# Performance work log

Hardware: AMD Instinct MI355X
Metric: run time of the kernel (lower is better)

## Reference

```python
import jax, jax.numpy as jnp
import numpy as np
from functools import partial

B, L, V = 64, 512, 20000
P, M = 150, 6          # total patterns, max pattern length
NEG = -1e9             # semiring zero (log-space)
END_STATES = np.repeat(np.array([3, 4, 5]), 50)  # pattern_len-1 per pattern


@jax.custom_vjp
def ste_heaviside(x):
    return (x > 0).astype(x.dtype)

def _ste_fwd(x):
    return ste_heaviside(x), None

def _ste_bwd(_, g):
    return (g,)  # straight-through identity (matches torch code path)

ste_heaviside.defvjp(_ste_fwd, _ste_bwd)


def setup_inputs() -> dict:
    key = jax.random.key(0)
    ks = jax.random.split(key, 8)
    return {
        "docs": jax.random.randint(ks[0], (B, L), 0, V),
        "doc_lens": jax.random.randint(ks[1], (B,), 1, L),
        "local_embeddings": jax.random.normal(ks[2], (300, V), jnp.float32),
        "diags": jax.random.normal(ks[3], (P * M, 300), jnp.float32) * 0.05,
        "bias": jax.random.normal(ks[4], (P * M, 1), jnp.float32) * 0.05,
        "wildcards": jax.random.normal(ks[5], (P, M - 1), jnp.float32) * 0.05,
        "ln_gamma": jnp.ones((P,), jnp.float32),
        "ln_beta": jnp.zeros((P,), jnp.float32),
        "linear_w": jax.random.normal(ks[6], (2, P), jnp.float32) * 0.05,
        "linear_b": jnp.zeros((2,), jnp.float32),
    }


def reference(docs, doc_lens, local_embeddings, diags, bias, wildcards,
              ln_gamma, ln_beta, linear_w, linear_b):
    end_states = jnp.asarray(END_STATES)                  # [P]
    pat_idx = jnp.arange(P)

    # transition matrices over local vocab, mapped into log-space semiring
    tm_vocab = jax.nn.log_sigmoid((diags @ local_embeddings + bias).T)  # [V, P*M]
    tm = tm_vocab[docs].reshape(B, L, P, M)               # [B,L,P,M]

    # wildcard transitions: semiring.times(one=0, log_sigmoid(wildcards))
    wild = jax.nn.log_sigmoid(wildcards)                  # [P, M-1]

    restart = jnp.zeros((B, P, 1), tm.dtype)              # semiring one
    hid0 = jnp.full((B, P, M), NEG, tm.dtype).at[:, :, 0].set(0.0)
    scores0 = jnp.full((B, P), NEG, tm.dtype)             # semiring zero

    def step(carry, inputs):
        hid, sc = carry
        t, tm_t = inputs                                  # tm_t: [B,P,M]
        main = jnp.concatenate([restart, hid[:, :, :-1] + tm_t[:, :, :-1]], axis=2)
        wildp = jnp.concatenate([restart, hid[:, :, :-1] + wild[None]], axis=2)
        hid = jnp.maximum(main, wildp)                    # semiring plus
        esv = hid[:, pat_idx, end_states]                 # [B,P]
        active = (doc_lens > t)[:, None]
        sc = jnp.where(active, jnp.maximum(sc, esv), sc)
        return (hid, sc), None

    xs = (jnp.arange(L), jnp.moveaxis(tm, 1, 0))          # [L], [L,B,P,M]
    (_, scores), _ = jax.lax.scan(step, (hid0, scores0), xs)

    scores = jnp.exp(scores)                              # from_semiring_to_outer
    mu = scores.mean(axis=-1, keepdims=True)
    var = scores.var(axis=-1, keepdims=True)
    norm = (scores - mu) * jax.lax.rsqrt(var + 1e-5) * ln_gamma + ln_beta
    binar = ste_heaviside(norm)
    return binar @ linear_w.T + linear_b
```

## Files before the change

### kernel.cpp

```cpp
#include <hip/hip_runtime.h>
#include <hip/hip_bf16.h>
#include <hip/hip_fp16.h>
#include <math.h>

#define B_   64
#define L_   512
#define V_   20000
#define P_   150
#define M_   6
#define KDIM 300
#define NOUT 750
#define CWS  752
#define NEGF (-1.0e9f)

#define BM 128
#define BN 128
#define BK 16
#define LDP 132

#define KP 320
#define NIT 10
#define NVG 157
#define NJ  6
#define TILE_U4 1024
#define SA 1024.0f
#define SB 16384.0f
#define INV24 (5.9604644775390625e-8f)

#define TCHUNK 32
#define NCHUNK (L_ / TCHUNK)
#define WARM   5
#define CS_STRIDE 160

typedef _Float16 f16x8 __attribute__((ext_vector_type(8)));
typedef float f32x16 __attribute__((ext_vector_type(16)));

__device__ __forceinline__ float logsigf(float x) {
    return fminf(x, 0.f) - log1pf(expf(-fabsf(x)));
}

__device__ __forceinline__ float logsigf_fast(float x) {
    return fminf(x, 0.f) - __logf(1.f + __expf(-fabsf(x)));
}

__device__ __forceinline__ void gload_lds16(const void* gp, void* lp) {
    __builtin_amdgcn_global_load_lds(
        (const __attribute__((address_space(1))) unsigned int*)gp,
        (__attribute__((address_space(3))) unsigned int*)lp, 16, 0, 0);
}


__global__ __launch_bounds__(256) void p1_split_a(
    const float* __restrict__ emb, uint4* __restrict__ a_t)
{
    __shared__ float T[64][132];
    const int t  = threadIdx.x;
    const int gx = blockIdx.x;
    const int ky = blockIdx.y;
    const int v0 = gx * 128;
    const int k0 = ky * 64;

    #pragma unroll
    for (int pass = 0; pass < 8; ++pass) {
        int flat = pass * 256 + t;
        int krow = flat >> 5;
        int c4   = (flat & 31) * 4;
        int kg   = k0 + krow;
        int v    = v0 + c4;
        float4 f = {0.f, 0.f, 0.f, 0.f};
        if (kg < KDIM && v + 3 < V_)
            f = *(const float4*)(emb + (size_t)kg * V_ + v);
        *(float4*)&T[krow][c4] = f;
    }
    __syncthreads();

    const int vv = t >> 1;
    const int kh = (t & 1) * 32;
    const int it = ky * 2 + (kh >> 5);
    const int v  = v0 + vv;
    if (v < V_) {
        union { ushort u[8]; uint4 q; } H[4], Lo[4];
        #pragma unroll
        for (int i = 0; i < 32; ++i) {
            float x = T[kh + i][vv] * SA;
            __half h = __float2half_rn(x);
            float rem = x - __half2float(h);
            H[i >> 3].u[i & 7]  = __half_as_ushort(h);
            Lo[i >> 3].u[i & 7] = __half_as_ushort(__float2half_rn(rem));
        }
        uint4* tile = a_t + ((size_t)gx * NIT + it) * TILE_U4;
        #pragma unroll
        for (int c = 0; c < 4; ++c) {
            tile[      c * 128 + vv] = H[c].q;
            tile[512 + c * 128 + vv] = Lo[c].q;
        }
    }
}

__global__ __launch_bounds__(256) void p2_split_b(
    const float* __restrict__ diags, uint4* __restrict__ b_t)
{
    const int bidx = blockIdx.x;
    const int it   = bidx % NIT;
    const int j    = bidx / NIT;
    const int t    = threadIdx.x;
    const int row  = t >> 1;
    const int qh   = (t & 1) * 2;
    const int n    = j * 128 + row;
    const bool nok = (n < NOUT);
    const int pm   = nok ? ((n / 5) * 6 + (n % 5)) : 0;
    uint4* tile = b_t + (size_t)bidx * TILE_U4;
    #pragma unroll
    for (int qq = 0; qq < 2; ++qq) {
        int q = qh + qq;
        union { ushort u[8]; uint4 v; } H, Lo;
        #pragma unroll
        for (int e = 0; e < 8; ++e) {
            int k = it * 32 + q * 8 + e;
            float x = (nok && k < KDIM) ? diags[(size_t)pm * KDIM + k] * SB : 0.f;
            __half h = __float2half_rn(x);
            float rem = x - __half2float(h);
            H.u[e]  = __half_as_ushort(h);
            Lo.u[e] = __half_as_ushort(__float2half_rn(rem));
        }
        tile[      q * 128 + row] = H.v;
        tile[512 + q * 128 + row] = Lo.v;
    }
}

__global__ __launch_bounds__(256, 3) void k1m_gemm(
    const uint4* __restrict__ a_t, const uint4* __restrict__ b_t,
    const float* __restrict__ bias, const float* __restrict__ wildc,
    float* __restrict__ cw)
{
    const int bid  = blockIdx.x;
    const int xcd  = bid & 7;
    const int slot = bid >> 3;
    const int g    = xcd + 8 * (slot / 6);
    const int j    = slot % 6;
    if (g >= NVG) return;

    __shared__ uint4 sm[4 * 512];
    const int t    = threadIdx.x;
    const int lane = t & 63;
    const int w    = t >> 6;
    const int wr   = w >> 1, wc = w & 1;
    const int v0   = g * 128;
    const int n0   = j * 128;

    const uint4* gsec = (w < 2)
        ? a_t + (size_t)g * NIT * TILE_U4 + w * 512
        : b_t + (size_t)j * NIT * TILE_U4 + (w - 2) * 512;

    const int fk16 = lane >> 5;
    const int fm   = lane & 31;

    f32x16 acc[2][2];
    #pragma unroll
    for (int i = 0; i < 2; ++i)
        #pragma unroll
        for (int jj = 0; jj < 2; ++jj)
            #pragma unroll
            for (int r = 0; r < 16; ++r) acc[i][jj][r] = 0.f;

    for (int it = 0; it < NIT; ++it) {
        const uint4* gp = gsec + (size_t)it * TILE_U4 + lane;
        #pragma unroll
        for (int i = 0; i < 8; ++i)
            gload_lds16(gp + i * 64, &sm[w * 512 + i * 64 + lane]);
        __syncthreads();

        #pragma unroll
        for (int s = 0; s < 2; ++s) {
            f16x8 A1[2], A2[2], B1[2], B2[2];
            const int q = s * 2 + fk16;
            #pragma unroll
            for (int ri = 0; ri < 2; ++ri) {
                A1[ri] = *(const f16x8*)&sm[(0 * 4 + q) * 128 + wr * 64 + ri * 32 + fm];
                A2[ri] = *(const f16x8*)&sm[(1 * 4 + q) * 128 + wr * 64 + ri * 32 + fm];
            }
            #pragma unroll
            for (int cj = 0; cj < 2; ++cj) {
                B1[cj] = *(const f16x8*)&sm[(2 * 4 + q) * 128 + wc * 64 + cj * 32 + fm];
                B2[cj] = *(const f16x8*)&sm[(3 * 4 + q) * 128 + wc * 64 + cj * 32 + fm];
            }
            #pragma unroll
            for (int ri = 0; ri < 2; ++ri)
                #pragma unroll
                for (int cj = 0; cj < 2; ++cj) {
                    acc[ri][cj] = __builtin_amdgcn_mfma_f32_32x32x16_f16(A1[ri], B1[cj], acc[ri][cj], 0, 0, 0);
                    acc[ri][cj] = __builtin_amdgcn_mfma_f32_32x32x16_f16(A1[ri], B2[cj], acc[ri][cj], 0, 0, 0);
                    acc[ri][cj] = __builtin_amdgcn_mfma_f32_32x32x16_f16(A2[ri], B1[cj], acc[ri][cj], 0, 0, 0);
                }
        }
        __syncthreads();
    }

    float biasv[2], lwv[2]; int ncol[2]; bool nok[2];
    #pragma unroll
    for (int cj = 0; cj < 2; ++cj) {
        int n = n0 + wc * 64 + cj * 32 + fm;
        ncol[cj] = n;
        nok[cj]  = (n < NOUT);
        int nc = nok[cj] ? n : 0;
        int pm = (nc / 5) * 6 + (nc % 5);
        biasv[cj] = bias[pm];
        lwv[cj]   = logsigf_fast(wildc[nc]);
    }
    #pragma unroll
    for (int ri = 0; ri < 2; ++ri) {
        int vbase = v0 + wr * 64 + ri * 32 + 4 * fk16;
        #pragma unroll
        for (int cj = 0; cj < 2; ++cj) {
            if (!nok[cj]) continue;
            #pragma unroll
            for (int r = 0; r < 16; ++r) {
                int v = vbase + (r & 3) + 8 * (r >> 2);
                if (v < V_) {
                    float val = acc[ri][cj][r] * INV24 + biasv[cj];
                    cw[(size_t)v * CWS + ncol[cj]] = fmaxf(logsigf_fast(val), lwv[cj]);
                }
            }
        }
    }
}


__global__ __launch_bounds__(256) void k1_gemm_cw(
    const float* __restrict__ emb,
    const float* __restrict__ diags,
    const float* __restrict__ bias,
    const float* __restrict__ wildc,
    float* __restrict__ cw)
{
    __shared__ float As[BK][LDP];
    __shared__ float Bs[BK][LDP];

    const int tid = threadIdx.x;
    const int v0 = blockIdx.x * BM;
    const int n0 = blockIdx.y * BN;
    const int tx = tid & 15;
    const int ty = tid >> 4;

    float acc[8][8];
    #pragma unroll
    for (int i = 0; i < 8; ++i)
        #pragma unroll
        for (int j = 0; j < 8; ++j) acc[i][j] = 0.f;

    const int a_k = tid >> 4;
    const int a_v = (tid & 15) * 8;
    const int b_n   = tid >> 1;
    const int b_kof = (tid & 1) * 8;

    int  brow;
    bool bval;
    {
        int n = n0 + b_n;
        bval = (n < NOUT);
        brow = bval ? ((n / 5) * 6 + (n % 5)) : 0;
    }

    for (int k0 = 0; k0 < KDIM; k0 += BK) {
        {
            float4 f0 = {0,0,0,0}, f1 = {0,0,0,0};
            int k = k0 + a_k;
            if (k < KDIM) {
                const float* src = emb + (size_t)k * V_ + v0 + a_v;
                if (v0 + a_v + 3 < V_) f0 = *(const float4*)src;
                if (v0 + a_v + 7 < V_) f1 = *(const float4*)(src + 4);
            }
            *(float4*)&As[a_k][a_v]     = f0;
            *(float4*)&As[a_k][a_v + 4] = f1;
        }
        {
            float4 f = {0,0,0,0}, g = {0,0,0,0};
            if (bval) {
                const float* src = diags + (size_t)brow * KDIM + k0 + b_kof;
                if (k0 + b_kof + 3 < KDIM) f = *(const float4*)src;
                if (k0 + b_kof + 7 < KDIM) g = *(const float4*)(src + 4);
            }
            Bs[b_kof + 0][b_n] = f.x;
            Bs[b_kof + 1][b_n] = f.y;
            Bs[b_kof + 2][b_n] = f.z;
            Bs[b_kof + 3][b_n] = f.w;
            Bs[b_kof + 4][b_n] = g.x;
            Bs[b_kof + 5][b_n] = g.y;
            Bs[b_kof + 6][b_n] = g.z;
            Bs[b_kof + 7][b_n] = g.w;
        }
        __syncthreads();
        #pragma unroll
        for (int k = 0; k < BK; ++k) {
            float4 a0 = *(const float4*)&As[k][tx * 4];
            float4 a1 = *(const float4*)&As[k][64 + tx * 4];
            float4 b0 = *(const float4*)&Bs[k][ty * 8];
            float4 b1 = *(const float4*)&Bs[k][ty * 8 + 4];
            float av[8] = {a0.x, a0.y, a0.z, a0.w, a1.x, a1.y, a1.z, a1.w};
            float bv[8] = {b0.x, b0.y, b0.z, b0.w, b1.x, b1.y, b1.z, b1.w};
            #pragma unroll
            for (int i = 0; i < 8; ++i)
                #pragma unroll
                for (int j = 0; j < 8; ++j)
                    acc[i][j] = fmaf(av[i], bv[j], acc[i][j]);
        }
        __syncthreads();
    }

    float biasv[8], lwv[8];
    #pragma unroll
    for (int j = 0; j < 8; ++j) {
        int n  = n0 + ty * 8 + j;
        int nc = (n < NOUT) ? n : 0;
        int pm = (nc / 5) * 6 + (nc % 5);
        biasv[j] = bias[pm];
        lwv[j]   = logsigf(wildc[nc]);
    }
    #pragma unroll
    for (int i = 0; i < 8; ++i) {
        int v = v0 + ((i < 4) ? (tx * 4 + i) : (64 + tx * 4 + (i - 4)));
        if (v >= V_) continue;
        float r[8];
        #pragma unroll
        for (int j = 0; j < 8; ++j)
            r[j] = fmaxf(logsigf(acc[i][j] + biasv[j]), lwv[j]);
        float* dst = cw + (size_t)v * CWS + n0 + ty * 8;
        if (n0 + ty * 8     < NOUT) *(float4*)dst       = make_float4(r[0], r[1], r[2], r[3]);
        if (n0 + ty * 8 + 4 < NOUT) *(float4*)(dst + 4) = make_float4(r[4], r[5], r[6], r[7]);
    }
}


__global__ __launch_bounds__(192) void k2_scan(
    const int* __restrict__ docs,
    const int* __restrict__ doc_lens,
    const float* __restrict__ cw,
    float* __restrict__ cs)
{
    const int ci = blockIdx.x;
    const int b  = blockIdx.y;
    const int t0 = ci * TCHUNK;
    const int ts = (t0 >= WARM) ? (t0 - WARM) : 0;
    const int dl = doc_lens[b];
    const int te = min(t0 + TCHUNK, dl);
    const int nt = te - ts;

    __shared__ int   toks[TCHUNK + WARM];
    __shared__ float rows[3][768];

    const int t    = threadIdx.x;
    const int lane = t & 63;
    const int w    = t >> 6;

    if (t < TCHUNK + WARM) {
        int tt = ts + t;
        toks[t] = docs[b * L_ + min(tt, L_ - 1)];
    }
    __syncthreads();

    const int p      = t;
    const int e      = (p < 50) ? 3 : (p < 100) ? 4 : 5;
    const int warm_n = t0 - ts;
    float h1 = NEGF, h2 = NEGF, h3 = NEGF, h4 = NEGF, h5 = NEGF, sc = NEGF;

    const int nrounds = (nt > 0) ? (nt + 2) / 3 : 0;
    for (int r = 0; r < nrounds; ++r) {
        {
            int idx = min(3 * r + w, nt - 1);
            const char* rowp = (const char*)(cw + (size_t)toks[idx] * CWS);
            char* lbase = (char*)&rows[w][0];
            #pragma unroll
            for (int jj = 0; jj < 3; ++jj)
                gload_lds16(rowp + jj * 1024 + lane * 16,
                            lbase + jj * 1024 + lane * 16);
        }
        __syncthreads();

        #pragma unroll
        for (int u = 0; u < 3; ++u) {
            int i2 = 3 * r + u;
            if (i2 >= nt) break;
            if (p < P_) {
                const float* rp = &rows[u][p * 5];
                float c0 = rp[0], c1 = rp[1], c2 = rp[2], c3 = rp[3], c4 = rp[4];
                h5 = h4 + c4;
                h4 = h3 + c3;
                h3 = h2 + c2;
                h2 = h1 + c1;
                h1 = c0;
                if (i2 >= warm_n) {
                    float esv = (e == 3) ? h3 : (e == 4) ? h4 : h5;
                    sc = fmaxf(sc, esv);
                }
            }
        }
        __syncthreads();
    }
    if (p < P_) cs[(size_t)(b * NCHUNK + ci) * CS_STRIDE + p] = sc;
}

__device__ __forceinline__ float block_sum192(float v, volatile float* red, int tid) {
    #pragma unroll
    for (int off = 32; off > 0; off >>= 1) v += __shfl_down(v, off, 64);
    __syncthreads();
    if ((tid & 63) == 0) red[tid >> 6] = v;
    __syncthreads();
    return red[0] + red[1] + red[2];
}

__global__ __launch_bounds__(192) void k3_final(
    const float* __restrict__ cs,
    const float* __restrict__ gamma,
    const float* __restrict__ beta,
    const float* __restrict__ lw,
    const float* __restrict__ lb,
    float* __restrict__ out)
{
    __shared__ float red[3];
    const int b   = blockIdx.x;
    const int tid = threadIdx.x;
    float s = 0.f;
    if (tid < P_) {
        float m = NEGF;
        const float* row = cs + (size_t)b * NCHUNK * CS_STRIDE + tid;
        #pragma unroll
        for (int ci = 0; ci < NCHUNK; ++ci) m = fmaxf(m, row[ci * CS_STRIDE]);
        s = expf(m);
    }
    float mu = block_sum192(s, red, tid) * (1.f / P_);
    float d  = (tid < P_) ? (s - mu) : 0.f;
    float var = block_sum192(d * d, red, tid) * (1.f / P_);
    float bin = 0.f;
    if (tid < P_) {
        float norm = (s - mu) * rsqrtf(var + 1e-5f) * gamma[tid] + beta[tid];
        bin = (norm > 0.f) ? 1.f : 0.f;
    }
    float o0 = block_sum192((tid < P_) ? bin * lw[tid]      : 0.f, red, tid);
    float o1 = block_sum192((tid < P_) ? bin * lw[P_ + tid] : 0.f, red, tid);
    if (tid == 0) {
        out[b * 2 + 0] = o0 + lb[0];
        out[b * 2 + 1] = o1 + lb[1];
    }
}

extern "C" void kernel_launch(void* const* d_in, const int* in_sizes, int n_in,
                              void* d_out, int out_size, void* d_ws, size_t ws_size,
                              hipStream_t stream)
{
    const int*   docs  = (const int*)  d_in[0];
    const int*   dlens = (const int*)  d_in[1];
    const float* emb   = (const float*)d_in[2];
    const float* diags = (const float*)d_in[3];
    const float* bias  = (const float*)d_in[4];
    const float* wildc = (const float*)d_in[5];
    const float* gamma = (const float*)d_in[6];
    const float* beta  = (const float*)d_in[7];
    const float* lw    = (const float*)d_in[8];
    const float* lb    = (const float*)d_in[9];
    float* out = (float*)d_out;

    const size_t cw_b = (size_t)V_ * CWS * 4;
    const size_t cs_b = (size_t)B_ * NCHUNK * CS_STRIDE * 4;
    const size_t at_b = (size_t)NVG * NIT * TILE_U4 * 16;
    const size_t bt_b = (size_t)NJ  * NIT * TILE_U4 * 16;
    const size_t need = cw_b + cs_b + at_b + bt_b;

    char* base = (char*)d_ws;
    float* cw = (float*)base;
    float* cs = (float*)(base + cw_b);
    uint4* at = (uint4*)(base + cw_b + cs_b);
    uint4* bt = (uint4*)(base + cw_b + cs_b + at_b);

    if (ws_size >= need) {
        p1_split_a<<<dim3(NVG, 5), 256, 0, stream>>>(emb, at);
        p2_split_b<<<NJ * NIT, 256, 0, stream>>>(diags, bt);
        k1m_gemm<<<960, 256, 0, stream>>>(at, bt, bias, wildc, cw);
    } else {
        dim3 g1((V_ + BM - 1) / BM, (NOUT + BN - 1) / BN);
        k1_gemm_cw<<<g1, 256, 0, stream>>>(emb, diags, bias, wildc, cw);
    }

    dim3 g2(NCHUNK, B_);
    k2_scan<<<g2, 192, 0, stream>>>(docs, dlens, cw, cs);
    k3_final<<<B_, 192, 0, stream>>>(cs, gamma, beta, lw, lb, out);
}
```

Baseline: 153.4 us.

## Merge split kernels into one launch and widen GEMM N-tile to 256

The two fp16 hi/lo split kernels are combined into a single launch with block-index dispatch, removing one kernel launch. The GEMM tile is widened from 128x128 to 128x256 output columns per block, so each A tile loaded into LDS is reused across twice as many columns and the grid halves from 960 to 480 blocks. This raises accumulator registers and LDS use per block (launch bounds lowered to 2 blocks per CU), and the last column-pair tile covers columns past 750 where work is partially masked.

Result: no change. 150.8 us (-1.7%).

```diff
diff --git a/kernel.cpp b/kernel.cpp
--- a/kernel.cpp
+++ b/kernel.cpp
@@ -50,85 +50,85 @@
 }
 
 
-__global__ __launch_bounds__(256) void p1_split_a(
-    const float* __restrict__ emb, uint4* __restrict__ a_t)
+__global__ __launch_bounds__(256) void p12_split(
+    const float* __restrict__ emb, const float* __restrict__ diags,
+    uint4* __restrict__ a_t, uint4* __restrict__ b_t)
 {
     __shared__ float T[64][132];
-    const int t  = threadIdx.x;
-    const int gx = blockIdx.x;
-    const int ky = blockIdx.y;
-    const int v0 = gx * 128;
-    const int k0 = ky * 64;
-
-    #pragma unroll
-    for (int pass = 0; pass < 8; ++pass) {
-        int flat = pass * 256 + t;
-        int krow = flat >> 5;
-        int c4   = (flat & 31) * 4;
-        int kg   = k0 + krow;
-        int v    = v0 + c4;
-        float4 f = {0.f, 0.f, 0.f, 0.f};
-        if (kg < KDIM && v + 3 < V_)
-            f = *(const float4*)(emb + (size_t)kg * V_ + v);
-        *(float4*)&T[krow][c4] = f;
-    }
-    __syncthreads();
-
-    const int vv = t >> 1;
-    const int kh = (t & 1) * 32;
-    const int it = ky * 2 + (kh >> 5);
-    const int v  = v0 + vv;
-    if (v < V_) {
-        union { ushort u[8]; uint4 q; } H[4], Lo[4];
-        #pragma unroll
-        for (int i = 0; i < 32; ++i) {
-            float x = T[kh + i][vv] * SA;
-            __half h = __float2half_rn(x);
-            float rem = x - __half2float(h);
-            H[i >> 3].u[i & 7]  = __half_as_ushort(h);
-            Lo[i >> 3].u[i & 7] = __half_as_ushort(__float2half_rn(rem));
-        }
-        uint4* tile = a_t + ((size_t)gx * NIT + it) * TILE_U4;
-        #pragma unroll
-        for (int c = 0; c < 4; ++c) {
-            tile[      c * 128 + vv] = H[c].q;
-            tile[512 + c * 128 + vv] = Lo[c].q;
-        }
-    }
-}
-
-__global__ __launch_bounds__(256) void p2_split_b(
-    const float* __restrict__ diags, uint4* __restrict__ b_t)
-{
-    const int bidx = blockIdx.x;
-    const int it   = bidx % NIT;
-    const int j    = bidx / NIT;
-    const int t    = threadIdx.x;
-    const int row  = t >> 1;
-    const int qh   = (t & 1) * 2;
-    const int n    = j * 128 + row;
-    const bool nok = (n < NOUT);
-    const int pm   = nok ? ((n / 5) * 6 + (n % 5)) : 0;
-    uint4* tile = b_t + (size_t)bidx * TILE_U4;
-    #pragma unroll
-    for (int qq = 0; qq < 2; ++qq) {
-        int q = qh + qq;
-        union { ushort u[8]; uint4 v; } H, Lo;
-        #pragma unroll
-        for (int e = 0; e < 8; ++e) {
-            int k = it * 32 + q * 8 + e;
-            float x = (nok && k < KDIM) ? diags[(size_t)pm * KDIM + k] * SB : 0.f;
-            __half h = __float2half_rn(x);
-            float rem = x - __half2float(h);
-            H.u[e]  = __half_as_ushort(h);
-            Lo.u[e] = __half_as_ushort(__float2half_rn(rem));
-        }
-        tile[      q * 128 + row] = H.v;
-        tile[512 + q * 128 + row] = Lo.v;
-    }
-}
-
-__global__ __launch_bounds__(256, 3) void k1m_gemm(
+    const int t   = threadIdx.x;
+    const int bid = blockIdx.x;
+
+    if (bid < NVG * 5) {
+        const int gx = bid % NVG;
+        const int ky = bid / NVG;
+        const int v0 = gx * 128;
+        const int k0 = ky * 64;
+
+        #pragma unroll
+        for (int pass = 0; pass < 8; ++pass) {
+            int flat = pass * 256 + t;
+            int krow = flat >> 5;
+            int c4   = (flat & 31) * 4;
+            int kg   = k0 + krow;
+            int v    = v0 + c4;
+            float4 f = {0.f, 0.f, 0.f, 0.f};
+            if (kg < KDIM && v + 3 < V_)
+                f = *(const float4*)(emb + (size_t)kg * V_ + v);
+            *(float4*)&T[krow][c4] = f;
+        }
+        __syncthreads();
+
+        const int vv = t >> 1;
+        const int kh = (t & 1) * 32;
+        const int it = ky * 2 + (kh >> 5);
+        const int v  = v0 + vv;
+        if (v < V_) {
+            union { ushort u[8]; uint4 q; } H[4], Lo[4];
+            #pragma unroll
+            for (int i = 0; i < 32; ++i) {
+                float x = T[kh + i][vv] * SA;
+                __half h = __float2half_rn(x);
+                float rem = x - __half2float(h);
+                H[i >> 3].u[i & 7]  = __half_as_ushort(h);
+                Lo[i >> 3].u[i & 7] = __half_as_ushort(__float2half_rn(rem));
+            }
+            uint4* tile = a_t + ((size_t)gx * NIT + it) * TILE_U4;
+            #pragma unroll
+            for (int c = 0; c < 4; ++c) {
+                tile[      c * 128 + vv] = H[c].q;
+                tile[512 + c * 128 + vv] = Lo[c].q;
+            }
+        }
+    } else {
+        const int bidx = bid - NVG * 5;
+        const int it   = bidx % NIT;
+        const int j    = bidx / NIT;
+        const int row  = t >> 1;
+        const int qh   = (t & 1) * 2;
+        const int n    = j * 128 + row;
+        const bool nok = (n < NOUT);
+        const int pm   = nok ? ((n / 5) * 6 + (n % 5)) : 0;
+        uint4* tile = b_t + (size_t)bidx * TILE_U4;
+        #pragma unroll
+        for (int qq = 0; qq < 2; ++qq) {
+            int q = qh + qq;
+            union { ushort u[8]; uint4 v; } H, Lo;
+            #pragma unroll
+            for (int e = 0; e < 8; ++e) {
+                int k = it * 32 + q * 8 + e;
+                float x = (nok && k < KDIM) ? diags[(size_t)pm * KDIM + k] * SB : 0.f;
+                __half h = __float2half_rn(x);
+                float rem = x - __half2float(h);
+                H.u[e]  = __half_as_ushort(h);
+                Lo.u[e] = __half_as_ushort(__float2half_rn(rem));
+            }
+            tile[      q * 128 + row] = H.v;
+            tile[512 + q * 128 + row] = Lo.v;
+        }
+    }
+}
+
+__global__ __launch_bounds__(256, 2) void k1m_gemm(
     const uint4* __restrict__ a_t, const uint4* __restrict__ b_t,
     const float* __restrict__ bias, const float* __restrict__ wildc,
     float* __restrict__ cw)
@@ -136,58 +136,67 @@
     const int bid  = blockIdx.x;
     const int xcd  = bid & 7;
     const int slot = bid >> 3;
-    const int g    = xcd + 8 * (slot / 6);
-    const int j    = slot % 6;
+    const int g    = xcd + 8 * (slot / 3);
+    const int jp   = slot % 3;
     if (g >= NVG) return;
 
-    __shared__ uint4 sm[4 * 512];
+    __shared__ uint4 sm[3072];
     const int t    = threadIdx.x;
     const int lane = t & 63;
     const int w    = t >> 6;
     const int wr   = w >> 1, wc = w & 1;
     const int v0   = g * 128;
-    const int n0   = j * 128;
-
-    const uint4* gsec = (w < 2)
-        ? a_t + (size_t)g * NIT * TILE_U4 + w * 512
-        : b_t + (size_t)j * NIT * TILE_U4 + (w - 2) * 512;
+    const int n0   = jp * 256;
 
     const int fk16 = lane >> 5;
     const int fm   = lane & 31;
 
-    f32x16 acc[2][2];
+    f32x16 acc[2][4];
     #pragma unroll
     for (int i = 0; i < 2; ++i)
         #pragma unroll
-        for (int jj = 0; jj < 2; ++jj)
+        for (int jj = 0; jj < 4; ++jj)
             #pragma unroll
             for (int r = 0; r < 16; ++r) acc[i][jj][r] = 0.f;
 
     for (int it = 0; it < NIT; ++it) {
-        const uint4* gp = gsec + (size_t)it * TILE_U4 + lane;
-        #pragma unroll
-        for (int i = 0; i < 8; ++i)
-            gload_lds16(gp + i * 64, &sm[w * 512 + i * 64 + lane]);
+        if (w < 2) {
+            const uint4* gp = a_t + ((size_t)g * NIT + it) * TILE_U4 + w * 512 + lane;
+            #pragma unroll
+            for (int i = 0; i < 8; ++i)
+                gload_lds16(gp + i * 64, &sm[w * 512 + i * 64 + lane]);
+        } else {
+            const int s = w - 2;
+            #pragma unroll
+            for (int jt = 0; jt < 2; ++jt) {
+                const uint4* gp = b_t + ((size_t)(2 * jp + jt) * NIT + it) * TILE_U4
+                                      + s * 512 + lane;
+                #pragma unroll
+                for (int i = 0; i < 8; ++i)
+                    gload_lds16(gp + i * 64,
+                                &sm[1024 + s * 1024 + jt * 512 + i * 64 + lane]);
+            }
+        }
         __syncthreads();
 
         #pragma unroll
         for (int s = 0; s < 2; ++s) {
-            f16x8 A1[2], A2[2], B1[2], B2[2];
+            f16x8 A1[2], A2[2], B1[4], B2[4];
             const int q = s * 2 + fk16;
             #pragma unroll
             for (int ri = 0; ri < 2; ++ri) {
-                A1[ri] = *(const f16x8*)&sm[(0 * 4 + q) * 128 + wr * 64 + ri * 32 + fm];
-                A2[ri] = *(const f16x8*)&sm[(1 * 4 + q) * 128 + wr * 64 + ri * 32 + fm];
-            }
-            #pragma unroll
-            for (int cj = 0; cj < 2; ++cj) {
-                B1[cj] = *(const f16x8*)&sm[(2 * 4 + q) * 128 + wc * 64 + cj * 32 + fm];
-                B2[cj] = *(const f16x8*)&sm[(3 * 4 + q) * 128 + wc * 64 + cj * 32 + fm];
+                A1[ri] = *(const f16x8*)&sm[        q * 128 + wr * 64 + ri * 32 + fm];
+                A2[ri] = *(const f16x8*)&sm[512   + q * 128 + wr * 64 + ri * 32 + fm];
+            }
+            #pragma unroll
+            for (int cj = 0; cj < 4; ++cj) {
+                B1[cj] = *(const f16x8*)&sm[1024 + wc * 512 + q * 128 + cj * 32 + fm];
+                B2[cj] = *(const f16x8*)&sm[2048 + wc * 512 + q * 128 + cj * 32 + fm];
             }
             #pragma unroll
             for (int ri = 0; ri < 2; ++ri)
                 #pragma unroll
-                for (int cj = 0; cj < 2; ++cj) {
+                for (int cj = 0; cj < 4; ++cj) {
                     acc[ri][cj] = __builtin_amdgcn_mfma_f32_32x32x16_f16(A1[ri], B1[cj], acc[ri][cj], 0, 0, 0);
                     acc[ri][cj] = __builtin_amdgcn_mfma_f32_32x32x16_f16(A1[ri], B2[cj], acc[ri][cj], 0, 0, 0);
                     acc[ri][cj] = __builtin_amdgcn_mfma_f32_32x32x16_f16(A2[ri], B1[cj], acc[ri][cj], 0, 0, 0);
@@ -196,10 +205,10 @@
         __syncthreads();
     }
 
-    float biasv[2], lwv[2]; int ncol[2]; bool nok[2];
-    #pragma unroll
-    for (int cj = 0; cj < 2; ++cj) {
-        int n = n0 + wc * 64 + cj * 32 + fm;
+    float biasv[4], lwv[4]; int ncol[4]; bool nok[4];
+    #pragma unroll
+    for (int cj = 0; cj < 4; ++cj) {
+        int n = n0 + wc * 128 + cj * 32 + fm;
         ncol[cj] = n;
         nok[cj]  = (n < NOUT);
         int nc = nok[cj] ? n : 0;
@@ -211,7 +220,7 @@
     for (int ri = 0; ri < 2; ++ri) {
         int vbase = v0 + wr * 64 + ri * 32 + 4 * fk16;
         #pragma unroll
-        for (int cj = 0; cj < 2; ++cj) {
+        for (int cj = 0; cj < 4; ++cj) {
             if (!nok[cj]) continue;
             #pragma unroll
             for (int r = 0; r < 16; ++r) {
@@ -472,9 +481,8 @@
     uint4* bt = (uint4*)(base + cw_b + cs_b + at_b);
 
     if (ws_size >= need) {
-        p1_split_a<<<dim3(NVG, 5), 256, 0, stream>>>(emb, at);
-        p2_split_b<<<NJ * NIT, 256, 0, stream>>>(diags, bt);
-        k1m_gemm<<<960, 256, 0, stream>>>(at, bt, bias, wildc, cw);
+        p12_split<<<NVG * 5 + NJ * NIT, 256, 0, stream>>>(emb, diags, at, bt);
+        k1m_gemm<<<480, 256, 0, stream>>>(at, bt, bias, wildc, cw);
     } else {
         dim3 g1((V_ + BM - 1) / BM, (NOUT + BN - 1) / BN);
         k1_gemm_cw<<<g1, 256, 0, stream>>>(emb, diags, bias, wildc, cw);
```

## Double-buffer GEMM LDS tiles and merge split kernels into one launch

Applied to the files above, without the earlier changes.

The two preprocessing kernels that split the embedding and diag matrices into fp16 hi/lo tiles are merged into one launch, with the block index choosing the role. This saves one kernel launch. The MFMA GEMM now double-buffers its LDS tiles: the next tile's global-to-LDS loads are issued before computing on the current one, leaving one barrier per iteration instead of two. LDS use doubles, so launch bounds drop from 3 to 2 blocks per SM, which may reduce occupancy.

Result: faster. 148.4 us (-3.3%).

```diff
diff --git a/kernel.cpp b/kernel.cpp
--- a/kernel.cpp
+++ b/kernel.cpp
@@ -50,85 +50,85 @@
 }
 
 
-__global__ __launch_bounds__(256) void p1_split_a(
-    const float* __restrict__ emb, uint4* __restrict__ a_t)
+__global__ __launch_bounds__(256) void p12_split(
+    const float* __restrict__ emb, const float* __restrict__ diags,
+    uint4* __restrict__ a_t, uint4* __restrict__ b_t)
 {
     __shared__ float T[64][132];
-    const int t  = threadIdx.x;
-    const int gx = blockIdx.x;
-    const int ky = blockIdx.y;
-    const int v0 = gx * 128;
-    const int k0 = ky * 64;
-
-    #pragma unroll
-    for (int pass = 0; pass < 8; ++pass) {
-        int flat = pass * 256 + t;
-        int krow = flat >> 5;
-        int c4   = (flat & 31) * 4;
-        int kg   = k0 + krow;
-        int v    = v0 + c4;
-        float4 f = {0.f, 0.f, 0.f, 0.f};
-        if (kg < KDIM && v + 3 < V_)
-            f = *(const float4*)(emb + (size_t)kg * V_ + v);
-        *(float4*)&T[krow][c4] = f;
-    }
-    __syncthreads();
-
-    const int vv = t >> 1;
-    const int kh = (t & 1) * 32;
-    const int it = ky * 2 + (kh >> 5);
-    const int v  = v0 + vv;
-    if (v < V_) {
-        union { ushort u[8]; uint4 q; } H[4], Lo[4];
-        #pragma unroll
-        for (int i = 0; i < 32; ++i) {
-            float x = T[kh + i][vv] * SA;
-            __half h = __float2half_rn(x);
-            float rem = x - __half2float(h);
-            H[i >> 3].u[i & 7]  = __half_as_ushort(h);
-            Lo[i >> 3].u[i & 7] = __half_as_ushort(__float2half_rn(rem));
-        }
-        uint4* tile = a_t + ((size_t)gx * NIT + it) * TILE_U4;
-        #pragma unroll
-        for (int c = 0; c < 4; ++c) {
-            tile[      c * 128 + vv] = H[c].q;
-            tile[512 + c * 128 + vv] = Lo[c].q;
-        }
-    }
-}
-
-__global__ __launch_bounds__(256) void p2_split_b(
-    const float* __restrict__ diags, uint4* __restrict__ b_t)
-{
-    const int bidx = blockIdx.x;
-    const int it   = bidx % NIT;
-    const int j    = bidx / NIT;
-    const int t    = threadIdx.x;
-    const int row  = t >> 1;
-    const int qh   = (t & 1) * 2;
-    const int n    = j * 128 + row;
-    const bool nok = (n < NOUT);
-    const int pm   = nok ? ((n / 5) * 6 + (n % 5)) : 0;
-    uint4* tile = b_t + (size_t)bidx * TILE_U4;
-    #pragma unroll
-    for (int qq = 0; qq < 2; ++qq) {
-        int q = qh + qq;
-        union { ushort u[8]; uint4 v; } H, Lo;
-        #pragma unroll
-        for (int e = 0; e < 8; ++e) {
-            int k = it * 32 + q * 8 + e;
-            float x = (nok && k < KDIM) ? diags[(size_t)pm * KDIM + k] * SB : 0.f;
-            __half h = __float2half_rn(x);
-            float rem = x - __half2float(h);
-            H.u[e]  = __half_as_ushort(h);
-            Lo.u[e] = __half_as_ushort(__float2half_rn(rem));
-        }
-        tile[      q * 128 + row] = H.v;
-        tile[512 + q * 128 + row] = Lo.v;
-    }
-}
-
-__global__ __launch_bounds__(256, 3) void k1m_gemm(
+    const int t   = threadIdx.x;
+    const int bid = blockIdx.x;
+
+    if (bid < NVG * 5) {
+        const int gx = bid % NVG;
+        const int ky = bid / NVG;
+        const int v0 = gx * 128;
+        const int k0 = ky * 64;
+
+        #pragma unroll
+        for (int pass = 0; pass < 8; ++pass) {
+            int flat = pass * 256 + t;
+            int krow = flat >> 5;
+            int c4   = (flat & 31) * 4;
+            int kg   = k0 + krow;
+            int v    = v0 + c4;
+            float4 f = {0.f, 0.f, 0.f, 0.f};
+            if (kg < KDIM && v + 3 < V_)
+                f = *(const float4*)(emb + (size_t)kg * V_ + v);
+            *(float4*)&T[krow][c4] = f;
+        }
+        __syncthreads();
+
+        const int vv = t >> 1;
+        const int kh = (t & 1) * 32;
+        const int it = ky * 2 + (kh >> 5);
+        const int v  = v0 + vv;
+        if (v < V_) {
+            union { ushort u[8]; uint4 q; } H[4], Lo[4];
+            #pragma unroll
+            for (int i = 0; i < 32; ++i) {
+                float x = T[kh + i][vv] * SA;
+                __half h = __float2half_rn(x);
+                float rem = x - __half2float(h);
+                H[i >> 3].u[i & 7]  = __half_as_ushort(h);
+                Lo[i >> 3].u[i & 7] = __half_as_ushort(__float2half_rn(rem));
+            }
+            uint4* tile = a_t + ((size_t)gx * NIT + it) * TILE_U4;
+            #pragma unroll
+            for (int c = 0; c < 4; ++c) {
+                tile[      c * 128 + vv] = H[c].q;
+                tile[512 + c * 128 + vv] = Lo[c].q;
+            }
+        }
+    } else {
+        const int bidx = bid - NVG * 5;
+        const int it   = bidx % NIT;
+        const int j    = bidx / NIT;
+        const int row  = t >> 1;
+        const int qh   = (t & 1) * 2;
+        const int n    = j * 128 + row;
+        const bool nok = (n < NOUT);
+        const int pm   = nok ? ((n / 5) * 6 + (n % 5)) : 0;
+        uint4* tile = b_t + (size_t)bidx * TILE_U4;
+        #pragma unroll
+        for (int qq = 0; qq < 2; ++qq) {
+            int q = qh + qq;
+            union { ushort u[8]; uint4 v; } H, Lo;
+            #pragma unroll
+            for (int e = 0; e < 8; ++e) {
+                int k = it * 32 + q * 8 + e;
+                float x = (nok && k < KDIM) ? diags[(size_t)pm * KDIM + k] * SB : 0.f;
+                __half h = __float2half_rn(x);
+                float rem = x - __half2float(h);
+                H.u[e]  = __half_as_ushort(h);
+                Lo.u[e] = __half_as_ushort(__float2half_rn(rem));
+            }
+            tile[      q * 128 + row] = H.v;
+            tile[512 + q * 128 + row] = Lo.v;
+        }
+    }
+}
+
+__global__ __launch_bounds__(256, 2) void k1m_gemm(
     const uint4* __restrict__ a_t, const uint4* __restrict__ b_t,
     const float* __restrict__ bias, const float* __restrict__ wildc,
     float* __restrict__ cw)
@@ -140,7 +140,7 @@
     const int j    = slot % 6;
     if (g >= NVG) return;
 
-    __shared__ uint4 sm[4 * 512];
+    __shared__ uint4 sm[2][2048];
     const int t    = threadIdx.x;
     const int lane = t & 63;
     const int w    = t >> 6;
@@ -163,26 +163,38 @@
             #pragma unroll
             for (int r = 0; r < 16; ++r) acc[i][jj][r] = 0.f;
 
+    {
+        const uint4* gp = gsec + lane;
+        #pragma unroll
+        for (int i = 0; i < 8; ++i)
+            gload_lds16(gp + i * 64, &sm[0][w * 512 + i * 64 + lane]);
+    }
+
+    int cur = 0;
     for (int it = 0; it < NIT; ++it) {
-        const uint4* gp = gsec + (size_t)it * TILE_U4 + lane;
-        #pragma unroll
-        for (int i = 0; i < 8; ++i)
-            gload_lds16(gp + i * 64, &sm[w * 512 + i * 64 + lane]);
-        __syncthreads();
-
+        __syncthreads();
+
+        if (it + 1 < NIT) {
+            const uint4* gp = gsec + (size_t)(it + 1) * TILE_U4 + lane;
+            #pragma unroll
+            for (int i = 0; i < 8; ++i)
+                gload_lds16(gp + i * 64, &sm[cur ^ 1][w * 512 + i * 64 + lane]);
+        }
+
+        const uint4* smc = sm[cur];
         #pragma unroll
         for (int s = 0; s < 2; ++s) {
             f16x8 A1[2], A2[2], B1[2], B2[2];
             const int q = s * 2 + fk16;
             #pragma unroll
             for (int ri = 0; ri < 2; ++ri) {
-                A1[ri] = *(const f16x8*)&sm[(0 * 4 + q) * 128 + wr * 64 + ri * 32 + fm];
-                A2[ri] = *(const f16x8*)&sm[(1 * 4 + q) * 128 + wr * 64 + ri * 32 + fm];
+                A1[ri] = *(const f16x8*)&smc[(0 * 4 + q) * 128 + wr * 64 + ri * 32 + fm];
+                A2[ri] = *(const f16x8*)&smc[(1 * 4 + q) * 128 + wr * 64 + ri * 32 + fm];
             }
             #pragma unroll
             for (int cj = 0; cj < 2; ++cj) {
-                B1[cj] = *(const f16x8*)&sm[(2 * 4 + q) * 128 + wc * 64 + cj * 32 + fm];
-                B2[cj] = *(const f16x8*)&sm[(3 * 4 + q) * 128 + wc * 64 + cj * 32 + fm];
+                B1[cj] = *(const f16x8*)&smc[(2 * 4 + q) * 128 + wc * 64 + cj * 32 + fm];
+                B2[cj] = *(const f16x8*)&smc[(3 * 4 + q) * 128 + wc * 64 + cj * 32 + fm];
             }
             #pragma unroll
             for (int ri = 0; ri < 2; ++ri)
@@ -193,7 +205,7 @@
                     acc[ri][cj] = __builtin_amdgcn_mfma_f32_32x32x16_f16(A2[ri], B1[cj], acc[ri][cj], 0, 0, 0);
                 }
         }
-        __syncthreads();
+        cur ^= 1;
     }
 
     float biasv[2], lwv[2]; int ncol[2]; bool nok[2];
@@ -472,8 +484,7 @@
     uint4* bt = (uint4*)(base + cw_b + cs_b + at_b);
 
     if (ws_size >= need) {
-        p1_split_a<<<dim3(NVG, 5), 256, 0, stream>>>(emb, at);
-        p2_split_b<<<NJ * NIT, 256, 0, stream>>>(diags, bt);
+        p12_split<<<NVG * 5 + NJ * NIT, 256, 0, stream>>>(emb, diags, at, bt);
         k1m_gemm<<<960, 256, 0, stream>>>(at, bt, bias, wildc, cw);
     } else {
         dim3 g1((V_ + BM - 1) / BM, (NOUT + BN - 1) / BN);
```
